# Performance work log

Hardware: AMD Instinct MI355X
Metric: run time of the kernel (lower is better)

Reference implementation:

```python
import jax, jax.numpy as jnp
import numpy as np

N = 100000
E = 3200000
NFEAT, NHID, NCLASS = 512, 256, 64
K = 10
ALPHA = 0.1


def setup_inputs() -> dict:
    key = jax.random.key(0)
    k1, k2, k3, k4, k5 = jax.random.split(key, 5)
    x = jax.random.normal(k1, (N, NFEAT), dtype=jnp.float32)
    edge_index = jax.random.randint(k2, (2, E), 0, N, dtype=jnp.int64)
    # Linear params (Kaiming-ish scale)
    W1 = jax.random.normal(k3, (NFEAT, NHID), dtype=jnp.float32) / np.sqrt(NFEAT)
    b1 = jnp.zeros((NHID,), dtype=jnp.float32)
    W2 = jax.random.normal(k4, (NHID, NCLASS), dtype=jnp.float32) / np.sqrt(NHID)
    b2 = jnp.zeros((NCLASS,), dtype=jnp.float32)
    # GPR coefficients: temp[k] = alpha*(1-alpha)^k, temp[K] = (1-alpha)^K
    temp = ALPHA * (1.0 - ALPHA) ** np.arange(K + 1)
    temp[-1] = (1.0 - ALPHA) ** K
    temp = jnp.asarray(temp, dtype=jnp.float32)
    return {"x": x, "edge_index": edge_index, "W1": W1, "b1": b1,
            "W2": W2, "b2": b2, "temp": temp}


def _gcn_norm(edge_index, num_nodes):
    # add self-loops, symmetric GCN normalization (PyG gcn_norm, edge_weight=1)
    loop = jnp.arange(num_nodes, dtype=edge_index.dtype)
    src = jnp.concatenate([edge_index[0], loop])
    dst = jnp.concatenate([edge_index[1], loop])
    deg = jnp.zeros((num_nodes,), dtype=jnp.float32).at[dst].add(1.0)
    dinv = jnp.where(deg > 0, jax.lax.rsqrt(deg), 0.0)
    norm = dinv[src] * dinv[dst]
    return src, dst, norm


def reference(x, edge_index, W1, b1, W2, b2, temp):
    n = x.shape[0]
    # eval mode: dropout is identity
    h = jax.nn.relu(x @ W1 + b1)
    h = h @ W2 + b2  # [N, nclass]
    src, dst, norm = _gcn_norm(edge_index, n)
    hidden = h * temp[0]
    for k in range(K):
        # one GCN-normalized hop: out[dst] += norm * h[src]
        h = jax.ops.segment_sum(norm[:, None] * h[src], dst, num_segments=n)
        hidden = hidden + temp[k + 1] * h
    return jax.nn.log_softmax(hidden, axis=1)
```

## Files before the change

kernel.cpp:

```cpp
#include <hip/hip_runtime.h>

#define N_NODES 100000
#define N_EDGES 3200000
#define NFEAT 512
#define NHID 256
#define NCLASS 64
#define KHOPS 10
#define SCAN_B 391

#define NBSHIFT 9
#define NBUCK 196
#define BCAP 20480
#define TILE 4096

typedef __bf16 bf16x8 __attribute__((ext_vector_type(8)));
typedef __bf16 bf16x4 __attribute__((ext_vector_type(4)));
typedef float f32x4 __attribute__((ext_vector_type(4)));


__global__ __launch_bounds__(256) void zero_deg_kernel(int* __restrict__ deg, int* __restrict__ bcursor) {
    int i = blockIdx.x * 256 + threadIdx.x;
    if (i < N_NODES) deg[i] = 0;
    if (blockIdx.x == 0 && threadIdx.x < NBUCK) bcursor[threadIdx.x] = 0;
}

__global__ __launch_bounds__(256) void deg_kernel(const int* __restrict__ ei, int* __restrict__ deg) {
    int e = blockIdx.x * 256 + threadIdx.x;
    if (e < N_EDGES) atomicAdd(&deg[ei[N_EDGES + e]], 1);
}

__global__ __launch_bounds__(256) void dinv_kernel(const int* __restrict__ deg, float* __restrict__ dinv) {
    int i = blockIdx.x * 256 + threadIdx.x;
    if (i < N_NODES) dinv[i] = rsqrtf((float)(deg[i] + 1));
}


__global__ __launch_bounds__(256) void radix1_kernel(const int* __restrict__ ei,
                                                     int* __restrict__ bcursor,
                                                     int2* __restrict__ breg) {
    __shared__ int2 stage[TILE];
    __shared__ int hist[NBUCK];
    __shared__ int base[NBUCK];
    __shared__ int offs[NBUCK];
    int t = threadIdx.x;
    int e0 = blockIdx.x * TILE;
    int n = N_EDGES - e0; if (n > TILE) n = TILE;
    for (int i = t; i < NBUCK; i += 256) { hist[i] = 0; offs[i] = 0; }
    __syncthreads();
    for (int i = t; i < n; i += 256) {
        int s = ei[e0 + i];
        int d = ei[N_EDGES + e0 + i];
        stage[i] = make_int2(s, d);
        atomicAdd(&hist[d >> NBSHIFT], 1);
    }
    __syncthreads();
    for (int i = t; i < NBUCK; i += 256)
        if (hist[i]) base[i] = atomicAdd(&bcursor[i], hist[i]);
    __syncthreads();
    for (int i = t; i < n; i += 256) {
        int2 e = stage[i];
        int b = e.y >> NBSHIFT;
        int slot = base[b] + atomicAdd(&offs[b], 1);
        if (slot < BCAP) breg[(size_t)b * BCAP + slot] = e;
    }
}


__global__ __launch_bounds__(256) void bucket_deg_kernel(const int2* __restrict__ breg,
                                                         const int* __restrict__ bcursor,
                                                         int* __restrict__ deg,
                                                         float* __restrict__ dinv) {
    __shared__ int cnt[512];
    int b = blockIdx.x;
    int t = threadIdx.x;
    cnt[t] = 0; cnt[t + 256] = 0;
    __syncthreads();
    int n = bcursor[b]; if (n > BCAP) n = BCAP;
    const int2* bp = breg + (size_t)b * BCAP;
    for (int i = t; i < n; i += 256)
        atomicAdd(&cnt[bp[i].y & 511], 1);
    __syncthreads();
    int d0 = b << NBSHIFT;
    for (int j = t; j < 512; j += 256) {
        int i = d0 + j;
        if (i < N_NODES) {
            int d = cnt[j];
            deg[i] = d;
            dinv[i] = rsqrtf((float)(d + 1));
        }
    }
}


__global__ __launch_bounds__(256) void scan1_kernel(const int* __restrict__ deg, int* __restrict__ partial) {
    __shared__ int red[256];
    int t = threadIdx.x;
    int i = blockIdx.x * 256 + t;
    red[t] = (i < N_NODES) ? deg[i] + 1 : 0;
    __syncthreads();
    for (int off = 128; off > 0; off >>= 1) {
        if (t < off) red[t] += red[t + off];
        __syncthreads();
    }
    if (t == 0) partial[blockIdx.x] = red[0];
}

__global__ __launch_bounds__(512) void scan2_kernel(int* __restrict__ partial) {
    __shared__ int s[512];
    int t = threadIdx.x;
    int v = (t < SCAN_B) ? partial[t] : 0;
    s[t] = v;
    __syncthreads();
    for (int off = 1; off < 512; off <<= 1) {
        int add = (t >= off) ? s[t - off] : 0;
        __syncthreads();
        s[t] += add;
        __syncthreads();
    }
    if (t < SCAN_B) partial[t] = s[t] - v;
}

__global__ __launch_bounds__(256) void scan3_kernel(const int* __restrict__ deg,
                                                    const int* __restrict__ partial,
                                                    int* __restrict__ row_ptr,
                                                    int* __restrict__ cursor) {
    __shared__ int s[256];
    int t = threadIdx.x;
    int i = blockIdx.x * 256 + t;
    int v = (i < N_NODES) ? deg[i] + 1 : 0;
    s[t] = v;
    __syncthreads();
    for (int off = 1; off < 256; off <<= 1) {
        int add = (t >= off) ? s[t - off] : 0;
        __syncthreads();
        s[t] += add;
        __syncthreads();
    }
    int excl = s[t] - v + partial[blockIdx.x];
    if (i < N_NODES) {
        row_ptr[i] = excl;
        cursor[i] = excl;
        if (i == N_NODES - 1) row_ptr[N_NODES] = excl + v;
    }
}


__global__ __launch_bounds__(256) void radix2_kernel(const int2* __restrict__ breg,
                                                     const int* __restrict__ bcursor,
                                                     const int* __restrict__ row_ptr,
                                                     int* __restrict__ esrc) {
    __shared__ int lcur[512];
    int b = blockIdx.x;
    int t = threadIdx.x;
    int d0 = b << NBSHIFT;
    int nn = N_NODES - d0; if (nn > 512) nn = 512;
    for (int j = t; j < nn; j += 256) {
        int rp = row_ptr[d0 + j];
        lcur[j] = rp + 1;
        esrc[rp] = d0 + j;
    }
    __syncthreads();
    int cnt = bcursor[b]; if (cnt > BCAP) cnt = BCAP;
    const int2* bp = breg + (size_t)b * BCAP;
    for (int i = t; i < cnt; i += 256) {
        int2 e = bp[i];
        int p = atomicAdd(&lcur[e.y - d0], 1);
        esrc[p] = e.x;
    }
}

__global__ __launch_bounds__(256) void fill_kernel(const int* __restrict__ ei,
                                                   int* __restrict__ cursor,
                                                   int* __restrict__ esrc) {
    int e = blockIdx.x * 256 + threadIdx.x;
    if (e < N_EDGES) {
        int s = ei[e], d = ei[N_EDGES + e];
        int p = atomicAdd(&cursor[d], 1);
        esrc[p] = s;
    } else if (e < N_EDGES + N_NODES) {
        int i = e - N_EDGES;
        int p = atomicAdd(&cursor[i], 1);
        esrc[p] = i;
    }
}


__global__ __launch_bounds__(256) void wprep_kernel(const float* __restrict__ W1,
                                                    const float* __restrict__ W2,
                                                    __bf16* __restrict__ w1t,
                                                    __bf16* __restrict__ w2t) {
    int i = blockIdx.x * 256 + threadIdx.x;
    if (i < NFEAT * NHID) {
        int n = i >> 9, k = i & 511;
        w1t[i] = (__bf16)W1[k * NHID + n];
    } else {
        int j = i - NFEAT * NHID;
        if (j < NHID * NCLASS) {
            int n = j >> 8, k = j & 255;
            w2t[j] = (__bf16)W2[k * NCLASS + n];
        }
    }
}


#define MT 128
#define KC 64
#define XP 72
#define WP 72
#define HP 264

__global__ __launch_bounds__(512, 4) void mlp_kernel(const float* __restrict__ x,
                                                     const __bf16* __restrict__ w1t,
                                                     const float* __restrict__ b1,
                                                     const __bf16* __restrict__ w2t,
                                                     const float* __restrict__ b2,
                                                     const float* __restrict__ temp,
                                                     const float* __restrict__ dinv,
                                                     __bf16* __restrict__ u0,
                                                     float* __restrict__ hidden) {
    __shared__ char smem[67584] __attribute__((aligned(16)));
    __bf16* xs  = (__bf16*)smem;
    __bf16* wt  = (__bf16*)(smem + 18432);
    __bf16* h1s = (__bf16*)smem;

    int t = threadIdx.x;
    int wv = t >> 6, lane = t & 63;
    int lrow = lane & 15;
    int quad = lane >> 4;
    int row0 = blockIdx.x * MT;
    int wm = (wv >> 2) * 64;
    int wn = (wv & 3) * 64;

    const float* xpt[2];
    int xr[2], xc8[2];
    #pragma unroll
    for (int it = 0; it < 2; ++it) {
        int j = it * 512 + t;
        int r = j >> 3, c8 = j & 7;
        int rr = row0 + r; if (rr >= N_NODES) rr = N_NODES - 1;
        xpt[it] = &x[(size_t)rr * NFEAT + c8 * 8];
        xr[it] = r; xc8[it] = c8;
    }
    float4 px[4];
    px[0] = *(const float4*)(xpt[0]);
    px[1] = *(const float4*)(xpt[0] + 4);
    px[2] = *(const float4*)(xpt[1]);
    px[3] = *(const float4*)(xpt[1] + 4);

    f32x4 acc[4][4] = {};
    #pragma unroll 1
    for (int kc = 0; kc < NFEAT; kc += KC) {
        __syncthreads();
        #pragma unroll
        for (int it = 0; it < 2; ++it) {
            float4 v0 = px[it * 2], v1 = px[it * 2 + 1];
            bf16x8 o = { (__bf16)v0.x, (__bf16)v0.y, (__bf16)v0.z, (__bf16)v0.w,
                         (__bf16)v1.x, (__bf16)v1.y, (__bf16)v1.z, (__bf16)v1.w };
            *(bf16x8*)&xs[xr[it] * XP + xc8[it] * 8] = o;
        }
        #pragma unroll
        for (int it = 0; it < 4; ++it) {
            int j = it * 512 + t;
            int n = j >> 3, c8 = j & 7;
            *(bf16x8*)&wt[n * WP + c8 * 8] = *(const bf16x8*)&w1t[(size_t)n * NFEAT + kc + c8 * 8];
        }
        __syncthreads();
        if (kc + KC < NFEAT) {
            px[0] = *(const float4*)(xpt[0] + kc + KC);
            px[1] = *(const float4*)(xpt[0] + kc + KC + 4);
            px[2] = *(const float4*)(xpt[1] + kc + KC);
            px[3] = *(const float4*)(xpt[1] + kc + KC + 4);
        }
        #pragma unroll
        for (int ks = 0; ks < 2; ++ks) {
            int kof = ks * 32 + quad * 8;
            bf16x8 a[4], b[4];
            #pragma unroll
            for (int mt = 0; mt < 4; ++mt)
                a[mt] = *(const bf16x8*)&xs[(wm + mt * 16 + lrow) * XP + kof];
            #pragma unroll
            for (int nt = 0; nt < 4; ++nt)
                b[nt] = *(const bf16x8*)&wt[(wn + nt * 16 + lrow) * WP + kof];
            #pragma unroll
            for (int mt = 0; mt < 4; ++mt)
                #pragma unroll
                for (int nt = 0; nt < 4; ++nt)
                    acc[mt][nt] = __builtin_amdgcn_mfma_f32_16x16x32_bf16(a[mt], b[nt], acc[mt][nt], 0, 0, 0);
        }
    }
    __syncthreads();
    #pragma unroll
    for (int nt = 0; nt < 4; ++nt) {
        int coln = wn + nt * 16 + lrow;
        float bb = b1[coln];
        #pragma unroll
        for (int mt = 0; mt < 4; ++mt) {
            int rbase = wm + mt * 16 + quad * 4;
            #pragma unroll
            for (int r = 0; r < 4; ++r) {
                float v = acc[mt][nt][r] + bb;
                h1s[(rbase + r) * HP + coln] = (__bf16)fmaxf(v, 0.f);
            }
        }
    }
    __syncthreads();
    int rg = (wv >> 1) * 32;
    int cg = (wv & 1) * 32;
    f32x4 acc2[2][2] = {};
    #pragma unroll
    for (int ks = 0; ks < 8; ++ks) {
        int kof = ks * 32 + quad * 8;
        bf16x8 a2[2], bv[2];
        #pragma unroll
        for (int m2 = 0; m2 < 2; ++m2)
            a2[m2] = *(const bf16x8*)&h1s[(rg + m2 * 16 + lrow) * HP + kof];
        #pragma unroll
        for (int nt = 0; nt < 2; ++nt)
            bv[nt] = *(const bf16x8*)&w2t[(size_t)(cg + nt * 16 + lrow) * NHID + kof];
        #pragma unroll
        for (int m2 = 0; m2 < 2; ++m2)
            #pragma unroll
            for (int nt = 0; nt < 2; ++nt)
                acc2[m2][nt] = __builtin_amdgcn_mfma_f32_16x16x32_bf16(a2[m2], bv[nt], acc2[m2][nt], 0, 0, 0);
    }
    float t0 = temp[0];
    #pragma unroll
    for (int m2 = 0; m2 < 2; ++m2) {
        #pragma unroll
        for (int nt = 0; nt < 2; ++nt) {
            int coln = cg + nt * 16 + lrow;
            float bb = b2[coln];
            #pragma unroll
            for (int r = 0; r < 4; ++r) {
                int row = row0 + rg + m2 * 16 + quad * 4 + r;
                if (row < N_NODES) {
                    float v = acc2[m2][nt][r] + bb;
                    size_t idx = (size_t)row * NCLASS + coln;
                    hidden[idx] = t0 * v;
                    u0[idx] = (__bf16)(dinv[row] * v);
                }
            }
        }
    }
}


__global__ __launch_bounds__(256) void prop_kernel(const __bf16* __restrict__ uin,
                                                   __bf16* __restrict__ uout,
                                                   float* __restrict__ hidden,
                                                   const int* __restrict__ row_ptr,
                                                   const int* __restrict__ esrc,
                                                   const float* __restrict__ dinv,
                                                   const float* __restrict__ temp,
                                                   int ktap) {
    int node = blockIdx.x * 4 + (threadIdx.x >> 6);
    int lane = threadIdx.x & 63;
    int oct = lane >> 3, fi8 = lane & 7;
    int beg = row_ptr[node], end = row_ptr[node + 1];
    const uint4* urow = (const uint4*)uin;
    float acc[8] = {};
    int nit = (end - beg + 7) >> 3;
    #pragma unroll 4
    for (int it = 0; it < nit; ++it) {
        int e = beg + it * 8 + oct;
        int ec = min(e, end - 1);
        int s = __builtin_nontemporal_load(&esrc[ec]);
        float m = (e < end) ? 1.f : 0.f;
        uint4 v = urow[(size_t)s * 8 + fi8];
        unsigned vv;
        vv = v.x;
        acc[0] = fmaf(m, __int_as_float(vv << 16), acc[0]);
        acc[1] = fmaf(m, __int_as_float(vv & 0xffff0000u), acc[1]);
        vv = v.y;
        acc[2] = fmaf(m, __int_as_float(vv << 16), acc[2]);
        acc[3] = fmaf(m, __int_as_float(vv & 0xffff0000u), acc[3]);
        vv = v.z;
        acc[4] = fmaf(m, __int_as_float(vv << 16), acc[4]);
        acc[5] = fmaf(m, __int_as_float(vv & 0xffff0000u), acc[5]);
        vv = v.w;
        acc[6] = fmaf(m, __int_as_float(vv << 16), acc[6]);
        acc[7] = fmaf(m, __int_as_float(vv & 0xffff0000u), acc[7]);
    }
    #pragma unroll
    for (int j = 0; j < 8; ++j) {
        acc[j] += __shfl_xor(acc[j], 8);
        acc[j] += __shfl_xor(acc[j], 16);
        acc[j] += __shfl_xor(acc[j], 32);
    }
    if (oct == 0) {
        float di = dinv[node];
        float d2 = di * di;
        float tk = temp[ktap] * di;
        union { __bf16 b[8]; uint4 u; } pk;
        #pragma unroll
        for (int j = 0; j < 8; ++j) pk.b[j] = (__bf16)(d2 * acc[j]);
        ((uint4*)uout)[(size_t)node * 8 + fi8] = pk.u;
        float* hp = hidden + (size_t)node * NCLASS + fi8 * 8;
        float4 a = *(float4*)hp, b = *(float4*)(hp + 4);
        a.x = fmaf(tk, acc[0], a.x); a.y = fmaf(tk, acc[1], a.y);
        a.z = fmaf(tk, acc[2], a.z); a.w = fmaf(tk, acc[3], a.w);
        b.x = fmaf(tk, acc[4], b.x); b.y = fmaf(tk, acc[5], b.y);
        b.z = fmaf(tk, acc[6], b.z); b.w = fmaf(tk, acc[7], b.w);
        *(float4*)hp = a; *(float4*)(hp + 4) = b;
    }
}


__global__ __launch_bounds__(256) void lsm_kernel(float* __restrict__ io) {
    int i = blockIdx.x * 4 + (threadIdx.x >> 6);
    int j = threadIdx.x & 63;
    float v = io[(size_t)i * 64 + j];
    float m = v;
    #pragma unroll
    for (int o = 32; o > 0; o >>= 1) m = fmaxf(m, __shfl_xor(m, o));
    float ex = expf(v - m);
    float s = ex;
    #pragma unroll
    for (int o = 32; o > 0; o >>= 1) s += __shfl_xor(s, o);
    io[(size_t)i * 64 + j] = v - m - logf(s);
}

extern "C" void kernel_launch(void* const* d_in, const int* in_sizes, int n_in,
                              void* d_out, int out_size, void* d_ws, size_t ws_size,
                              hipStream_t stream) {
    const float* x    = (const float*)d_in[0];
    const int*   ei   = (const int*)d_in[1];
    const float* W1   = (const float*)d_in[2];
    const float* b1   = (const float*)d_in[3];
    const float* W2   = (const float*)d_in[4];
    const float* b2   = (const float*)d_in[5];
    const float* temp = (const float*)d_in[6];
    float* out = (float*)d_out;

    char* ws = (char*)d_ws;
    size_t off = 0;
    auto alloc = [&](size_t bytes) -> void* {
        void* p = ws + off;
        off = (off + bytes + 255) & ~(size_t)255;
        return p;
    };
    int*    deg     = (int*)alloc((size_t)N_NODES * 4);
    float*  dinv    = (float*)alloc((size_t)N_NODES * 4);
    int*    row_ptr = (int*)alloc((size_t)(N_NODES + 1) * 4);
    int*    cursor  = (int*)alloc((size_t)N_NODES * 4);
    int*    partial = (int*)alloc((size_t)SCAN_B * 4);
    int*    bcursor = (int*)alloc((size_t)NBUCK * 4);
    int*    esrc    = (int*)alloc((size_t)(N_EDGES + N_NODES) * 4);
    __bf16* ub0     = (__bf16*)alloc((size_t)N_NODES * NCLASS * 2);
    __bf16* ub1     = (__bf16*)alloc((size_t)N_NODES * NCLASS * 2);
    __bf16* w1t     = (__bf16*)alloc((size_t)NFEAT * NHID * 2);
    __bf16* w2t     = (__bf16*)alloc((size_t)NHID * NCLASS * 2);
    size_t breg_bytes = (size_t)NBUCK * BCAP * 8;
    bool use_radix = (off + breg_bytes <= ws_size);
    int2* breg = use_radix ? (int2*)alloc(breg_bytes) : (int2*)0;

    zero_deg_kernel<<<(N_NODES + 255) / 256, 256, 0, stream>>>(deg, bcursor);
    if (use_radix) {
        radix1_kernel<<<(N_EDGES + TILE - 1) / TILE, 256, 0, stream>>>(ei, bcursor, breg);
        bucket_deg_kernel<<<NBUCK, 256, 0, stream>>>(breg, bcursor, deg, dinv);
        scan1_kernel<<<SCAN_B, 256, 0, stream>>>(deg, partial);
        scan2_kernel<<<1, 512, 0, stream>>>(partial);
        scan3_kernel<<<SCAN_B, 256, 0, stream>>>(deg, partial, row_ptr, cursor);
        radix2_kernel<<<NBUCK, 256, 0, stream>>>(breg, bcursor, row_ptr, esrc);
    } else {
        deg_kernel<<<(N_EDGES + 255) / 256, 256, 0, stream>>>(ei, deg);
        dinv_kernel<<<(N_NODES + 255) / 256, 256, 0, stream>>>(deg, dinv);
        scan1_kernel<<<SCAN_B, 256, 0, stream>>>(deg, partial);
        scan2_kernel<<<1, 512, 0, stream>>>(partial);
        scan3_kernel<<<SCAN_B, 256, 0, stream>>>(deg, partial, row_ptr, cursor);
        fill_kernel<<<(N_EDGES + N_NODES + 255) / 256, 256, 0, stream>>>(ei, cursor, esrc);
    }
    wprep_kernel<<<(NFEAT * NHID + NHID * NCLASS + 255) / 256, 256, 0, stream>>>(W1, W2, w1t, w2t);

    mlp_kernel<<<(N_NODES + MT - 1) / MT, 512, 0, stream>>>(x, w1t, b1, w2t, b2, temp, dinv, ub0, out);

    __bf16* cur = ub0;
    __bf16* nxt = ub1;
    for (int k = 0; k < KHOPS; ++k) {
        prop_kernel<<<N_NODES / 4, 256, 0, stream>>>(cur, nxt, out, row_ptr, esrc, dinv, temp, k + 1);
        __bf16* tswap = cur; cur = nxt; nxt = tswap;
    }

    lsm_kernel<<<N_NODES / 4, 256, 0, stream>>>(out);
}
```

Measured before the change: 1.055 ms.

## Store all hop outputs in bf16 and accumulate weighted sum in final kernel

Instead of each propagation hop doing a read-modify-write of the fp32 hidden accumulator, every hop's bf16 output is kept in its own slice of a (K+1)-deep buffer. A new finale kernel sums the temp-weighted hops, rescales by 1/dinv, and applies log_softmax. This removes 2x fp32 hidden traffic per hop, trading it for one bf16 read of all hops at the end, plus more workspace and a lower-precision accumulation path (the bf16-stored scaled values, divided back by dinv).

```diff
diff --git a/kernel.cpp b/kernel.cpp
--- a/kernel.cpp
+++ b/kernel.cpp
@@ -214,10 +214,8 @@
                                                      const float* __restrict__ b1,
                                                      const __bf16* __restrict__ w2t,
                                                      const float* __restrict__ b2,
-                                                     const float* __restrict__ temp,
                                                      const float* __restrict__ dinv,
-                                                     __bf16* __restrict__ u0,
-                                                     float* __restrict__ hidden) {
+                                                     __bf16* __restrict__ u0) {
     __shared__ char smem[67584] __attribute__((aligned(16)));
     __bf16* xs  = (__bf16*)smem;
     __bf16* wt  = (__bf16*)(smem + 18432);
@@ -323,7 +321,6 @@
             for (int nt = 0; nt < 2; ++nt)
                 acc2[m2][nt] = __builtin_amdgcn_mfma_f32_16x16x32_bf16(a2[m2], bv[nt], acc2[m2][nt], 0, 0, 0);
     }
-    float t0 = temp[0];
     #pragma unroll
     for (int m2 = 0; m2 < 2; ++m2) {
         #pragma unroll
@@ -335,9 +332,7 @@
                 int row = row0 + rg + m2 * 16 + quad * 4 + r;
                 if (row < N_NODES) {
                     float v = acc2[m2][nt][r] + bb;
-                    size_t idx = (size_t)row * NCLASS + coln;
-                    hidden[idx] = t0 * v;
-                    u0[idx] = (__bf16)(dinv[row] * v);
+                    u0[(size_t)row * NCLASS + coln] = (__bf16)(dinv[row] * v);
                 }
             }
         }
@@ -347,12 +342,9 @@
 
 __global__ __launch_bounds__(256) void prop_kernel(const __bf16* __restrict__ uin,
                                                    __bf16* __restrict__ uout,
-                                                   float* __restrict__ hidden,
                                                    const int* __restrict__ row_ptr,
                                                    const int* __restrict__ esrc,
-                                                   const float* __restrict__ dinv,
-                                                   const float* __restrict__ temp,
-                                                   int ktap) {
+                                                   const float* __restrict__ dinv) {
     int node = blockIdx.x * 4 + (threadIdx.x >> 6);
     int lane = threadIdx.x & 63;
     int oct = lane >> 3, fi8 = lane & 7;
@@ -390,26 +382,29 @@
     if (oct == 0) {
         float di = dinv[node];
         float d2 = di * di;
-        float tk = temp[ktap] * di;
         union { __bf16 b[8]; uint4 u; } pk;
         #pragma unroll
         for (int j = 0; j < 8; ++j) pk.b[j] = (__bf16)(d2 * acc[j]);
         ((uint4*)uout)[(size_t)node * 8 + fi8] = pk.u;
-        float* hp = hidden + (size_t)node * NCLASS + fi8 * 8;
-        float4 a = *(float4*)hp, b = *(float4*)(hp + 4);
-        a.x = fmaf(tk, acc[0], a.x); a.y = fmaf(tk, acc[1], a.y);
-        a.z = fmaf(tk, acc[2], a.z); a.w = fmaf(tk, acc[3], a.w);
-        b.x = fmaf(tk, acc[4], b.x); b.y = fmaf(tk, acc[5], b.y);
-        b.z = fmaf(tk, acc[6], b.z); b.w = fmaf(tk, acc[7], b.w);
-        *(float4*)hp = a; *(float4*)(hp + 4) = b;
-    }
-}
-
-
-__global__ __launch_bounds__(256) void lsm_kernel(float* __restrict__ io) {
-    int i = blockIdx.x * 4 + (threadIdx.x >> 6);
+    }
+}
+
+
+__global__ __launch_bounds__(256) void finale_kernel(const __bf16* __restrict__ ubuf,
+                                                     const float* __restrict__ dinv,
+                                                     const float* __restrict__ temp,
+                                                     float* __restrict__ out) {
+    int node = blockIdx.x * 4 + (threadIdx.x >> 6);
     int j = threadIdx.x & 63;
-    float v = io[(size_t)i * 64 + j];
+    const unsigned short* ub = (const unsigned short*)ubuf;
+    float acc = 0.f;
+    #pragma unroll
+    for (int k = 0; k <= KHOPS; ++k) {
+        unsigned short us = __builtin_nontemporal_load(
+            &ub[(size_t)k * N_NODES * NCLASS + (size_t)node * NCLASS + j]);
+        acc = fmaf(temp[k], __int_as_float((unsigned)us << 16), acc);
+    }
+    float v = acc / dinv[node];
     float m = v;
     #pragma unroll
     for (int o = 32; o > 0; o >>= 1) m = fmaxf(m, __shfl_xor(m, o));
@@ -417,7 +412,7 @@
     float s = ex;
     #pragma unroll
     for (int o = 32; o > 0; o >>= 1) s += __shfl_xor(s, o);
-    io[(size_t)i * 64 + j] = v - m - logf(s);
+    out[(size_t)node * 64 + j] = v - m - logf(s);
 }
 
 extern "C" void kernel_launch(void* const* d_in, const int* in_sizes, int n_in,
@@ -446,8 +441,7 @@
     int*    partial = (int*)alloc((size_t)SCAN_B * 4);
     int*    bcursor = (int*)alloc((size_t)NBUCK * 4);
     int*    esrc    = (int*)alloc((size_t)(N_EDGES + N_NODES) * 4);
-    __bf16* ub0     = (__bf16*)alloc((size_t)N_NODES * NCLASS * 2);
-    __bf16* ub1     = (__bf16*)alloc((size_t)N_NODES * NCLASS * 2);
+    __bf16* ubuf    = (__bf16*)alloc((size_t)(KHOPS + 1) * N_NODES * NCLASS * 2);
     __bf16* w1t     = (__bf16*)alloc((size_t)NFEAT * NHID * 2);
     __bf16* w2t     = (__bf16*)alloc((size_t)NHID * NCLASS * 2);
     size_t breg_bytes = (size_t)NBUCK * BCAP * 8;
@@ -472,14 +466,14 @@
     }
     wprep_kernel<<<(NFEAT * NHID + NHID * NCLASS + 255) / 256, 256, 0, stream>>>(W1, W2, w1t, w2t);
 
-    mlp_kernel<<<(N_NODES + MT - 1) / MT, 512, 0, stream>>>(x, w1t, b1, w2t, b2, temp, dinv, ub0, out);
-
-    __bf16* cur = ub0;
-    __bf16* nxt = ub1;
+    mlp_kernel<<<(N_NODES + MT - 1) / MT, 512, 0, stream>>>(x, w1t, b1, w2t, b2, dinv, ubuf);
+
+    const size_t ustride = (size_t)N_NODES * NCLASS;
     for (int k = 0; k < KHOPS; ++k) {
-        prop_kernel<<<N_NODES / 4, 256, 0, stream>>>(cur, nxt, out, row_ptr, esrc, dinv, temp, k + 1);
-        __bf16* tswap = cur; cur = nxt; nxt = tswap;
-    }
-
-    lsm_kernel<<<N_NODES / 4, 256, 0, stream>>>(out);
-}
+        prop_kernel<<<N_NODES / 4, 256, 0, stream>>>(ubuf + (size_t)k * ustride,
+                                                     ubuf + (size_t)(k + 1) * ustride,
+                                                     row_ptr, esrc, dinv);
+    }
+
+    finale_kernel<<<N_NODES / 4, 256, 0, stream>>>(ubuf, dinv, temp, out);
+}
```

After: 995.1 us, median of 2. 1.06x faster.
